# Kernel tuning notes

Measured on AMD Instinct MI355X. Metric: run time of the kernel, lower is better.

The kernel has to match this reference:

```python
import jax, jax.numpy as jnp
import numpy as np

INPUT_CHANNELS = 3

def setup_inputs() -> dict:
    key = jax.random.key(0)
    kx, ky = jax.random.split(key)
    x = jax.random.normal(kx, (8, 4096, 3), dtype=jnp.float32)
    y = jax.random.normal(ky, (8, 4096, 3), dtype=jnp.float32)
    return {"x": x, "y": y}

def reference(x, y):
    # Match torch: truncate both clouds to common num_points and input_channels.
    num_points = min(x.shape[1], y.shape[1])
    x = x[:, :num_points, :INPUT_CHANNELS]
    y = y[:, :num_points, :INPUT_CHANNELS]
    # pdist[b, i, j] = ||x_i||^2 + ||y_j||^2 - 2 x_i . y_j  (squared Euclidean)
    x2 = jnp.sum(x * x, axis=-1)          # [B, N]
    y2 = jnp.sum(y * y, axis=-1)          # [B, N]
    zz = jnp.einsum('bic,bjc->bij', x, y) # [B, N, N]
    pdist = x2[:, :, None] + y2[:, None, :] - 2.0 * zz
    # min over i (dim 1): nearest x for each y; min over j (dim 2): nearest y for each x
    loss = jnp.mean(jnp.min(pdist, axis=1)) + jnp.mean(jnp.min(pdist, axis=2))
    return loss * 0.005
```

## Files before the change

### kernel.cpp

```cpp
#include <hip/hip_runtime.h>

#define NPTS 4096
#define NB   8
#define TOT  (2 * NB * NPTS)

typedef __attribute__((ext_vector_type(8)))  short          bf16x8;
typedef __attribute__((ext_vector_type(8)))  unsigned short u16x8;
typedef __attribute__((ext_vector_type(16))) float          f32x16;

__device__ __forceinline__ unsigned short bf16_rne(float f) {
    unsigned u = __float_as_uint(f);
    u += 0x7FFFu + ((u >> 16) & 1u);
    return (unsigned short)(u >> 16);
}
__device__ __forceinline__ float bf16_f(unsigned short s) {
    return __uint_as_float(((unsigned)s) << 16);
}


__global__ __launch_bounds__(256, 2) void chamfer_mfma(
    const float* __restrict__ x, const float* __restrict__ y,
    float* __restrict__ smaxp, float* __restrict__ out)
{
    __shared__ unsigned short sB[16384];
    __shared__ float buf[4][64][33];

    const int bid  = blockIdx.x;
    const int dirb = bid >> 5;
    const int sub  = bid & 31;
    const int iblk = sub >> 2;
    const int jq   = sub & 3;

    const int tid = threadIdx.x;
    const int w   = tid >> 6;
    const int l   = tid & 63;
    const int g   = l >> 5;
    const int pos = l & 31;

    if (bid == 0 && tid == 0) *out = 0.f;

    const float* Araw = (dirb < 8) ? x + (size_t)dirb * NPTS * 3
                                   : y + (size_t)(dirb - 8) * NPTS * 3;
    const int bcid = dirb ^ 8;
    const float* Braw = (bcid < 8) ? x + (size_t)bcid * NPTS * 3
                                   : y + (size_t)(bcid - 8) * NPTS * 3;

    #pragma unroll
    for (int k = 0; k < 4; ++k) {
        int p = tid + k * 256;
        const float* src = Braw + (size_t)(jq * 1024 + p) * 3;
        float c0 = src[0], c1 = src[1], c2 = src[2];
        float h  = -0.5f * (c0 * c0 + c1 * c1 + c2 * c2);
        unsigned short h0 = bf16_rne(c0), h1 = bf16_rne(c1), h2 = bf16_rne(c2);
        unsigned short l0 = bf16_rne(c0 - bf16_f(h0));
        unsigned short l1 = bf16_rne(c1 - bf16_f(h1));
        unsigned short l2 = bf16_rne(c2 - bf16_f(h2));
        unsigned short hh = bf16_rne(h);
        unsigned short hl = bf16_rne(h - bf16_f(hh));
        u16x8 blo, bhi;
        blo[0]=h0; blo[1]=h1; blo[2]=h2; blo[3]=h0; blo[4]=h1; blo[5]=h2; blo[6]=l0; blo[7]=l1;
        bhi[0]=l2; bhi[1]=hh; bhi[2]=hl; bhi[3]=0; bhi[4]=0; bhi[5]=0; bhi[6]=0; bhi[7]=0;
        int u = p >> 5, ppos = p & 31;
        char* dst = (char*)sB + (size_t)u * 1024 + (size_t)ppos * 16;
        *(u16x8*)dst         = blo;
        *(u16x8*)(dst + 512) = bhi;
    }

    const int it0 = iblk * 16 + w * 4;
    bf16x8 afr[4];
    #pragma unroll
    for (int t = 0; t < 4; ++t) {
        const float* ap = Araw + (size_t)((it0 + t) * 32 + pos) * 3;
        float c0 = ap[0], c1 = ap[1], c2 = ap[2];
        unsigned short h0 = bf16_rne(c0), h1 = bf16_rne(c1), h2 = bf16_rne(c2);
        unsigned short l0 = bf16_rne(c0 - bf16_f(h0));
        unsigned short l1 = bf16_rne(c1 - bf16_f(h1));
        unsigned short l2 = bf16_rne(c2 - bf16_f(h2));
        const short ONE = (short)0x3F80;
        bf16x8 alo, ahi;
        alo[0]=(short)h0; alo[1]=(short)h1; alo[2]=(short)h2; alo[3]=(short)l0;
        alo[4]=(short)l1; alo[5]=(short)l2; alo[6]=(short)h0; alo[7]=(short)h1;
        ahi[0]=(short)h2; ahi[1]=ONE; ahi[2]=ONE; ahi[3]=0;
        ahi[4]=0; ahi[5]=0; ahi[6]=0; ahi[7]=0;
        #pragma unroll
        for (int e = 0; e < 8; ++e) afr[t][e] = g ? ahi[e] : alo[e];
    }

    __syncthreads();

    f32x16 zc;
    #pragma unroll
    for (int r = 0; r < 16; ++r) zc[r] = 0.f;

    f32x16 run[4];
    #pragma unroll
    for (int t = 0; t < 4; ++t)
        #pragma unroll
        for (int r = 0; r < 16; ++r) run[t][r] = -3.0e38f;

    f32x16 p0, p1;
    #pragma unroll
    for (int r = 0; r < 16; ++r) { p0[r] = -3.0e38f; p1[r] = -3.0e38f; }

    const char* Bq = (const char*)sB + (size_t)g * 512 + (size_t)pos * 16;

    bf16x8 cb0 = *(const bf16x8*)(Bq);
    bf16x8 cb1 = *(const bf16x8*)(Bq + 1024);
    bf16x8 cb2 = *(const bf16x8*)(Bq + 2048);
    bf16x8 cb3 = *(const bf16x8*)(Bq + 3072);

#define STAGE(T, B0, B1, RP)                                                    \
    {                                                                           \
        f32x16 d0 = __builtin_amdgcn_mfma_f32_32x32x16_bf16(afr[T], B0, zc, 0, 0, 0); \
        f32x16 d1 = __builtin_amdgcn_mfma_f32_32x32x16_bf16(afr[T], B1, zc, 0, 0, 0); \
        _Pragma("unroll")                                                       \
        for (int r = 0; r < 16; ++r)                                            \
            run[RP][r] = fmaxf(fmaxf(p0[r], p1[r]), run[RP][r]);                \
        p0 = d0; p1 = d1;                                                       \
    }

    #pragma unroll 1
    for (int j = 0; j < 32; j += 4) {
        bf16x8 nb0, nb1, nb2, nb3;
        if (j < 28) {
            const char* Bn = Bq + (size_t)(j + 4) * 1024;
            nb0 = *(const bf16x8*)(Bn);
            nb1 = *(const bf16x8*)(Bn + 1024);
            nb2 = *(const bf16x8*)(Bn + 2048);
            nb3 = *(const bf16x8*)(Bn + 3072);
        }
        STAGE(0, cb0, cb1, 3)
        STAGE(1, cb0, cb1, 0)
        STAGE(2, cb0, cb1, 1)
        STAGE(3, cb0, cb1, 2)
        STAGE(0, cb2, cb3, 3)
        STAGE(1, cb2, cb3, 0)
        STAGE(2, cb2, cb3, 1)
        STAGE(3, cb2, cb3, 2)
        if (j < 28) { cb0 = nb0; cb1 = nb1; cb2 = nb2; cb3 = nb3; }
    }
#undef STAGE

    #pragma unroll
    for (int r = 0; r < 16; ++r)
        run[3][r] = fmaxf(fmaxf(p0[r], p1[r]), run[3][r]);

    const int slotbase = (((dirb * 8 + iblk) * 4 + jq) << 9);
    #pragma unroll
    for (int ph = 0; ph < 2; ++ph) {
        if (ph) __syncthreads();
        #pragma unroll
        for (int tl = 0; tl < 2; ++tl) {
            const int t = 2 * ph + tl;
            #pragma unroll
            for (int r = 0; r < 16; ++r) {
                int rowin = (r & 3) + 8 * (r >> 2) + 4 * g;
                buf[w][tl * 32 + rowin][pos] = run[t][r];
            }
        }
        __syncthreads();

        float m = buf[w][l][0];
        #pragma unroll
        for (int k = 1; k < 32; ++k) m = fmaxf(m, buf[w][l][k]);
        smaxp[slotbase + w * 128 + ph * 64 + l] = m;
    }
}

__global__ __launch_bounds__(256) void reduce_kernel(
    const float* __restrict__ smaxp,
    const float* __restrict__ x, const float* __restrict__ y,
    float* __restrict__ out)
{
    const int stride = 64 * 256;
    int tid = blockIdx.x * 256 + threadIdx.x;
    float s = 0.f;
    for (int k = tid; k < TOT; k += stride) {
        int cid = k >> 12, ri = k & 4095;
        int iblk = ri >> 9, rem = ri & 511;
        const float* base = smaxp + (((cid * 8 + iblk) * 4) << 9) + rem;
        float m = fmaxf(fmaxf(base[0], base[512]),
                        fmaxf(base[1024], base[1536]));
        const float* ap = (cid < 8) ? x + ((size_t)cid * NPTS + ri) * 3
                                    : y + ((size_t)(cid - 8) * NPTS + ri) * 3;
        float a0 = ap[0], a1 = ap[1], a2 = ap[2];
        s += m - 0.5f * (a0 * a0 + a1 * a1 + a2 * a2);
    }

    #pragma unroll
    for (int off = 32; off > 0; off >>= 1)
        s += __shfl_down(s, off);

    __shared__ float redb[4];
    const int lane = threadIdx.x & 63, wave = threadIdx.x >> 6;
    if (lane == 0) redb[wave] = s;
    __syncthreads();
    if (threadIdx.x == 0) {
        float t = redb[0] + redb[1] + redb[2] + redb[3];
        atomicAdd(out, t * (-2.0f * 0.005f / 32768.f));
    }
}

extern "C" void kernel_launch(void* const* d_in, const int* in_sizes, int n_in,
                              void* d_out, int out_size, void* d_ws, size_t ws_size,
                              hipStream_t stream) {
    const float* x = (const float*)d_in[0];
    const float* y = (const float*)d_in[1];
    float* out = (float*)d_out;

    float* smaxp = (float*)d_ws;

    chamfer_mfma<<<dim3(512), dim3(256), 0, stream>>>(x, y, smaxp, out);
    reduce_kernel<<<dim3(64), dim3(256), 0, stream>>>(smaxp, x, y, out);
}
```

Before: 66.49 us.

## Give each block the full B cloud and fold row-min and sum into one kernel

Each block now stages all 4096 B points (128 KB of dynamic LDS) instead of a quarter, so the per-row max over j finishes inside the block. That block also adds the norm term and reduces to one partial, which removes the smaxp workspace round trip and the cross-quarter max in the second kernel. The grid shrinks from 512 to 256 blocks, each wave holds 2 A tiles instead of 4, and a single-block final reduce writes the output directly instead of using an atomic. The cost is lower occupancy (1 block per CU with 128 KB of LDS, 256 blocks total), less reuse of each B fragment across A tiles, and a longer serial staging phase per block.

```diff
diff --git a/kernel.cpp b/kernel.cpp
--- a/kernel.cpp
+++ b/kernel.cpp
@@ -2,7 +2,6 @@
 
 #define NPTS 4096
 #define NB   8
-#define TOT  (2 * NB * NPTS)
 
 typedef __attribute__((ext_vector_type(8)))  short          bf16x8;
 typedef __attribute__((ext_vector_type(8)))  unsigned short u16x8;
@@ -18,18 +17,18 @@
 }
 
 
-__global__ __launch_bounds__(256, 2) void chamfer_mfma(
+__global__ __launch_bounds__(256, 1) void chamfer_fused(
     const float* __restrict__ x, const float* __restrict__ y,
-    float* __restrict__ smaxp, float* __restrict__ out)
+    float* __restrict__ partials)
 {
-    __shared__ unsigned short sB[16384];
-    __shared__ float buf[4][64][33];
+    extern __shared__ char smem[];
+    unsigned short* sB = (unsigned short*)smem;
+    float (*buf)[64][33] = (float (*)[64][33])smem;
+    __shared__ float redb[4];
 
     const int bid  = blockIdx.x;
-    const int dirb = bid >> 5;
-    const int sub  = bid & 31;
-    const int iblk = sub >> 2;
-    const int jq   = sub & 3;
+    const int dirb = bid >> 4;
+    const int ib2  = bid & 15;
 
     const int tid = threadIdx.x;
     const int w   = tid >> 6;
@@ -37,8 +36,6 @@
     const int g   = l >> 5;
     const int pos = l & 31;
 
-    if (bid == 0 && tid == 0) *out = 0.f;
-
     const float* Araw = (dirb < 8) ? x + (size_t)dirb * NPTS * 3
                                    : y + (size_t)(dirb - 8) * NPTS * 3;
     const int bcid = dirb ^ 8;
@@ -46,9 +43,9 @@
                                    : y + (size_t)(bcid - 8) * NPTS * 3;
 
     #pragma unroll
-    for (int k = 0; k < 4; ++k) {
-        int p = tid + k * 256;
-        const float* src = Braw + (size_t)(jq * 1024 + p) * 3;
+    for (int k = 0; k < 16; ++k) {
+        int p = k * 256 + tid;
+        const float* src = Braw + (size_t)p * 3;
         float c0 = src[0], c1 = src[1], c2 = src[2];
         float h  = -0.5f * (c0 * c0 + c1 * c1 + c2 * c2);
         unsigned short h0 = bf16_rne(c0), h1 = bf16_rne(c1), h2 = bf16_rne(c2);
@@ -66,10 +63,10 @@
         *(u16x8*)(dst + 512) = bhi;
     }
 
-    const int it0 = iblk * 16 + w * 4;
-    bf16x8 afr[4];
-    #pragma unroll
-    for (int t = 0; t < 4; ++t) {
+    const int it0 = ib2 * 8 + w * 2;
+    bf16x8 afr[2];
+    #pragma unroll
+    for (int t = 0; t < 2; ++t) {
         const float* ap = Araw + (size_t)((it0 + t) * 32 + pos) * 3;
         float c0 = ap[0], c1 = ap[1], c2 = ap[2];
         unsigned short h0 = bf16_rne(c0), h1 = bf16_rne(c1), h2 = bf16_rne(c2);
@@ -92,9 +89,9 @@
     #pragma unroll
     for (int r = 0; r < 16; ++r) zc[r] = 0.f;
 
-    f32x16 run[4];
-    #pragma unroll
-    for (int t = 0; t < 4; ++t)
+    f32x16 run[2];
+    #pragma unroll
+    for (int t = 0; t < 2; ++t)
         #pragma unroll
         for (int r = 0; r < 16; ++r) run[t][r] = -3.0e38f;
 
@@ -120,73 +117,62 @@
     }
 
     #pragma unroll 1
-    for (int j = 0; j < 32; j += 4) {
+    for (int j = 0; j < 128; j += 4) {
         bf16x8 nb0, nb1, nb2, nb3;
-        if (j < 28) {
+        if (j < 124) {
             const char* Bn = Bq + (size_t)(j + 4) * 1024;
             nb0 = *(const bf16x8*)(Bn);
             nb1 = *(const bf16x8*)(Bn + 1024);
             nb2 = *(const bf16x8*)(Bn + 2048);
             nb3 = *(const bf16x8*)(Bn + 3072);
         }
-        STAGE(0, cb0, cb1, 3)
+        STAGE(0, cb0, cb1, 1)
         STAGE(1, cb0, cb1, 0)
-        STAGE(2, cb0, cb1, 1)
-        STAGE(3, cb0, cb1, 2)
-        STAGE(0, cb2, cb3, 3)
+        STAGE(0, cb2, cb3, 1)
         STAGE(1, cb2, cb3, 0)
-        STAGE(2, cb2, cb3, 1)
-        STAGE(3, cb2, cb3, 2)
-        if (j < 28) { cb0 = nb0; cb1 = nb1; cb2 = nb2; cb3 = nb3; }
+        if (j < 124) { cb0 = nb0; cb1 = nb1; cb2 = nb2; cb3 = nb3; }
     }
 #undef STAGE
 
     #pragma unroll
     for (int r = 0; r < 16; ++r)
-        run[3][r] = fmaxf(fmaxf(p0[r], p1[r]), run[3][r]);
-
-    const int slotbase = (((dirb * 8 + iblk) * 4 + jq) << 9);
-    #pragma unroll
-    for (int ph = 0; ph < 2; ++ph) {
-        if (ph) __syncthreads();
+        run[1][r] = fmaxf(fmaxf(p0[r], p1[r]), run[1][r]);
+
+    __syncthreads();
+
+    #pragma unroll
+    for (int tl = 0; tl < 2; ++tl) {
         #pragma unroll
-        for (int tl = 0; tl < 2; ++tl) {
-            const int t = 2 * ph + tl;
-            #pragma unroll
-            for (int r = 0; r < 16; ++r) {
-                int rowin = (r & 3) + 8 * (r >> 2) + 4 * g;
-                buf[w][tl * 32 + rowin][pos] = run[t][r];
-            }
+        for (int r = 0; r < 16; ++r) {
+            int rowin = (r & 3) + 8 * (r >> 2) + 4 * g;
+            buf[w][tl * 32 + rowin][pos] = run[tl][r];
         }
-        __syncthreads();
-
-        float m = buf[w][l][0];
-        #pragma unroll
-        for (int k = 1; k < 32; ++k) m = fmaxf(m, buf[w][l][k]);
-        smaxp[slotbase + w * 128 + ph * 64 + l] = m;
-    }
-}
-
-__global__ __launch_bounds__(256) void reduce_kernel(
-    const float* __restrict__ smaxp,
-    const float* __restrict__ x, const float* __restrict__ y,
-    float* __restrict__ out)
+    }
+    __syncthreads();
+
+    float m = buf[w][l][0];
+    #pragma unroll
+    for (int k = 1; k < 32; ++k) m = fmaxf(m, buf[w][l][k]);
+
+    int row = ib2 * 256 + w * 64 + l;
+    const float* ap = Araw + (size_t)row * 3;
+    float a0 = ap[0], a1 = ap[1], a2 = ap[2];
+    float s = m - 0.5f * (a0 * a0 + a1 * a1 + a2 * a2);
+
+    #pragma unroll
+    for (int off = 32; off > 0; off >>= 1)
+        s += __shfl_down(s, off);
+
+    if (l == 0) redb[w] = s;
+    __syncthreads();
+    if (tid == 0)
+        partials[bid] = redb[0] + redb[1] + redb[2] + redb[3];
+}
+
+__global__ __launch_bounds__(256) void final_reduce(
+    const float* __restrict__ partials, float* __restrict__ out)
 {
-    const int stride = 64 * 256;
-    int tid = blockIdx.x * 256 + threadIdx.x;
-    float s = 0.f;
-    for (int k = tid; k < TOT; k += stride) {
-        int cid = k >> 12, ri = k & 4095;
-        int iblk = ri >> 9, rem = ri & 511;
-        const float* base = smaxp + (((cid * 8 + iblk) * 4) << 9) + rem;
-        float m = fmaxf(fmaxf(base[0], base[512]),
-                        fmaxf(base[1024], base[1536]));
-        const float* ap = (cid < 8) ? x + ((size_t)cid * NPTS + ri) * 3
-                                    : y + ((size_t)(cid - 8) * NPTS + ri) * 3;
-        float a0 = ap[0], a1 = ap[1], a2 = ap[2];
-        s += m - 0.5f * (a0 * a0 + a1 * a1 + a2 * a2);
-    }
-
+    float s = partials[threadIdx.x];
     #pragma unroll
     for (int off = 32; off > 0; off >>= 1)
         s += __shfl_down(s, off);
@@ -196,8 +182,8 @@
     if (lane == 0) redb[wave] = s;
     __syncthreads();
     if (threadIdx.x == 0) {
-        float t = redb[0] + redb[1] + redb[2] + redb[3];
-        atomicAdd(out, t * (-2.0f * 0.005f / 32768.f));
+        out[0] = (redb[0] + redb[1] + redb[2] + redb[3])
+                 * (-2.0f * 0.005f / 32768.f);
     }
 }
 
@@ -208,8 +194,8 @@
     const float* y = (const float*)d_in[1];
     float* out = (float*)d_out;
 
-    float* smaxp = (float*)d_ws;
-
-    chamfer_mfma<<<dim3(512), dim3(256), 0, stream>>>(x, y, smaxp, out);
-    reduce_kernel<<<dim3(64), dim3(256), 0, stream>>>(smaxp, x, y, out);
-}
+    float* partials = (float*)d_ws;
+
+    chamfer_fused<<<dim3(256), dim3(256), 131072, stream>>>(x, y, partials);
+    final_reduce<<<dim3(1), dim3(256), 0, stream>>>(partials, out);
+}
```

New measurement: 76.41 us. 1.15x slower.

## Halve per-wave row tiles, double grid, alias LDS and drop software pipelining

Applied to the files above, without the earlier changes.

Each wave now handles 2 row tiles instead of 4, and the grid doubles to 1024 blocks. Launch bounds rise to 4 blocks per SM, and the B staging buffer and reduction buffer share one LDS allocation so more blocks fit per CU. The register-level prefetch of B fragments and the delayed-max pipeline are removed in favour of a simpler loop, and the reduce kernel's indexing is adjusted to the new partial layout. The goal is more parallelism and occupancy across 256 CUs. The cost is that each B load from LDS is now reused for fewer MFMAs, and MFMA latency has less explicit hiding within each wave.

```diff
diff --git a/kernel.cpp b/kernel.cpp
--- a/kernel.cpp
+++ b/kernel.cpp
@@ -1,8 +1,7 @@
 #include <hip/hip_runtime.h>
 
 #define NPTS 4096
-#define NB   8
-#define TOT  (2 * NB * NPTS)
+#define TOT  (2 * 8 * NPTS)
 
 typedef __attribute__((ext_vector_type(8)))  short          bf16x8;
 typedef __attribute__((ext_vector_type(8)))  unsigned short u16x8;
@@ -18,16 +17,17 @@
 }
 
 
-__global__ __launch_bounds__(256, 2) void chamfer_mfma(
+__global__ __launch_bounds__(256, 4) void chamfer_mfma(
     const float* __restrict__ x, const float* __restrict__ y,
     float* __restrict__ smaxp, float* __restrict__ out)
 {
-    __shared__ unsigned short sB[16384];
-    __shared__ float buf[4][64][33];
+    __shared__ __align__(16) char smem[33792];
+    unsigned short* sB = (unsigned short*)smem;
+    float (*buf)[64][33] = (float (*)[64][33])smem;
 
     const int bid  = blockIdx.x;
-    const int dirb = bid >> 5;
-    const int sub  = bid & 31;
+    const int dirb = bid >> 6;
+    const int sub  = bid & 63;
     const int iblk = sub >> 2;
     const int jq   = sub & 3;
 
@@ -47,7 +47,7 @@
 
     #pragma unroll
     for (int k = 0; k < 4; ++k) {
-        int p = tid + k * 256;
+        int p = k * 256 + tid;
         const float* src = Braw + (size_t)(jq * 1024 + p) * 3;
         float c0 = src[0], c1 = src[1], c2 = src[2];
         float h  = -0.5f * (c0 * c0 + c1 * c1 + c2 * c2);
@@ -66,10 +66,10 @@
         *(u16x8*)(dst + 512) = bhi;
     }
 
-    const int it0 = iblk * 16 + w * 4;
-    bf16x8 afr[4];
+    const int it0 = iblk * 8 + w * 2;
+    bf16x8 afr[2];
     #pragma unroll
-    for (int t = 0; t < 4; ++t) {
+    for (int t = 0; t < 2; ++t) {
         const float* ap = Araw + (size_t)((it0 + t) * 32 + pos) * 3;
         float c0 = ap[0], c1 = ap[1], c2 = ap[2];
         unsigned short h0 = bf16_rne(c0), h1 = bf16_rne(c1), h2 = bf16_rne(c2);
@@ -92,79 +92,55 @@
     #pragma unroll
     for (int r = 0; r < 16; ++r) zc[r] = 0.f;
 
-    f32x16 run[4];
+    f32x16 run[2];
     #pragma unroll
-    for (int t = 0; t < 4; ++t)
+    for (int t = 0; t < 2; ++t)
         #pragma unroll
         for (int r = 0; r < 16; ++r) run[t][r] = -3.0e38f;
 
-    f32x16 p0, p1;
-    #pragma unroll
-    for (int r = 0; r < 16; ++r) { p0[r] = -3.0e38f; p1[r] = -3.0e38f; }
-
     const char* Bq = (const char*)sB + (size_t)g * 512 + (size_t)pos * 16;
 
-    bf16x8 cb0 = *(const bf16x8*)(Bq);
-    bf16x8 cb1 = *(const bf16x8*)(Bq + 1024);
-    bf16x8 cb2 = *(const bf16x8*)(Bq + 2048);
-    bf16x8 cb3 = *(const bf16x8*)(Bq + 3072);
-
-#define STAGE(T, B0, B1, RP)                                                    \
+#define JPAIR(T, B0, B1)                                                        \
     {                                                                           \
         f32x16 d0 = __builtin_amdgcn_mfma_f32_32x32x16_bf16(afr[T], B0, zc, 0, 0, 0); \
         f32x16 d1 = __builtin_amdgcn_mfma_f32_32x32x16_bf16(afr[T], B1, zc, 0, 0, 0); \
         _Pragma("unroll")                                                       \
         for (int r = 0; r < 16; ++r)                                            \
-            run[RP][r] = fmaxf(fmaxf(p0[r], p1[r]), run[RP][r]);                \
-        p0 = d0; p1 = d1;                                                       \
+            run[T][r] = fmaxf(fmaxf(d0[r], d1[r]), run[T][r]);                  \
     }
 
     #pragma unroll 1
     for (int j = 0; j < 32; j += 4) {
-        bf16x8 nb0, nb1, nb2, nb3;
-        if (j < 28) {
-            const char* Bn = Bq + (size_t)(j + 4) * 1024;
-            nb0 = *(const bf16x8*)(Bn);
-            nb1 = *(const bf16x8*)(Bn + 1024);
-            nb2 = *(const bf16x8*)(Bn + 2048);
-            nb3 = *(const bf16x8*)(Bn + 3072);
-        }
-        STAGE(0, cb0, cb1, 3)
-        STAGE(1, cb0, cb1, 0)
-        STAGE(2, cb0, cb1, 1)
-        STAGE(3, cb0, cb1, 2)
-        STAGE(0, cb2, cb3, 3)
-        STAGE(1, cb2, cb3, 0)
-        STAGE(2, cb2, cb3, 1)
-        STAGE(3, cb2, cb3, 2)
-        if (j < 28) { cb0 = nb0; cb1 = nb1; cb2 = nb2; cb3 = nb3; }
+        const char* Bn = Bq + (size_t)j * 1024;
+        bf16x8 cb0 = *(const bf16x8*)(Bn);
+        bf16x8 cb1 = *(const bf16x8*)(Bn + 1024);
+        bf16x8 cb2 = *(const bf16x8*)(Bn + 2048);
+        bf16x8 cb3 = *(const bf16x8*)(Bn + 3072);
+        JPAIR(0, cb0, cb1)
+        JPAIR(1, cb0, cb1)
+        JPAIR(0, cb2, cb3)
+        JPAIR(1, cb2, cb3)
     }
-#undef STAGE
+#undef JPAIR
+
+    __syncthreads();
 
     #pragma unroll
-    for (int r = 0; r < 16; ++r)
-        run[3][r] = fmaxf(fmaxf(p0[r], p1[r]), run[3][r]);
+    for (int tl = 0; tl < 2; ++tl) {
+        #pragma unroll
+        for (int r = 0; r < 16; ++r) {
+            int rowin = (r & 3) + 8 * (r >> 2) + 4 * g;
+            buf[w][tl * 32 + rowin][pos] = run[tl][r];
+        }
+    }
+    __syncthreads();
 
-    const int slotbase = (((dirb * 8 + iblk) * 4 + jq) << 9);
+    float m = buf[w][l][0];
     #pragma unroll
-    for (int ph = 0; ph < 2; ++ph) {
-        if (ph) __syncthreads();
-        #pragma unroll
-        for (int tl = 0; tl < 2; ++tl) {
-            const int t = 2 * ph + tl;
-            #pragma unroll
-            for (int r = 0; r < 16; ++r) {
-                int rowin = (r & 3) + 8 * (r >> 2) + 4 * g;
-                buf[w][tl * 32 + rowin][pos] = run[t][r];
-            }
-        }
-        __syncthreads();
+    for (int k = 1; k < 32; ++k) m = fmaxf(m, buf[w][l][k]);
 
-        float m = buf[w][l][0];
-        #pragma unroll
-        for (int k = 1; k < 32; ++k) m = fmaxf(m, buf[w][l][k]);
-        smaxp[slotbase + w * 128 + ph * 64 + l] = m;
-    }
+    const int slotbase = (((dirb * 16 + iblk) * 4 + jq) << 8);
+    smaxp[slotbase + w * 64 + l] = m;
 }
 
 __global__ __launch_bounds__(256) void reduce_kernel(
@@ -177,10 +153,10 @@
     float s = 0.f;
     for (int k = tid; k < TOT; k += stride) {
         int cid = k >> 12, ri = k & 4095;
-        int iblk = ri >> 9, rem = ri & 511;
-        const float* base = smaxp + (((cid * 8 + iblk) * 4) << 9) + rem;
-        float m = fmaxf(fmaxf(base[0], base[512]),
-                        fmaxf(base[1024], base[1536]));
+        int iblk = ri >> 8, rem = ri & 255;
+        const float* base = smaxp + (((cid * 16 + iblk) * 4) << 8) + rem;
+        float m = fmaxf(fmaxf(base[0], base[256]),
+                        fmaxf(base[512], base[768]));
         const float* ap = (cid < 8) ? x + ((size_t)cid * NPTS + ri) * 3
                                     : y + ((size_t)(cid - 8) * NPTS + ri) * 3;
         float a0 = ap[0], a1 = ap[1], a2 = ap[2];
@@ -210,6 +186,6 @@
 
     float* smaxp = (float*)d_ws;
 
-    chamfer_mfma<<<dim3(512), dim3(256), 0, stream>>>(x, y, smaxp, out);
+    chamfer_mfma<<<dim3(1024), dim3(256), 0, stream>>>(x, y, smaxp, out);
     reduce_kernel<<<dim3(64), dim3(256), 0, stream>>>(smaxp, x, y, out);
 }
```

Result: slower. 71.29 us (+7.2%).
